# Performance work log

Hardware: AMD Instinct MI355X
Metric: run time of the kernel (lower is better)

Reference implementation:

```python
import jax, jax.numpy as jnp
import numpy as np

B, T, D = 4, 4096, 1024
HD = 64              # head_dim
H = D // HD          # n_heads = 16
C = 64               # chunk_size (T % C == 0)


def setup_inputs() -> dict:
    key = jax.random.key(0)
    k1, k2, k3 = jax.random.split(key, 3)
    out = jax.random.normal(k1, (B, T, D), jnp.float32)
    # Linear(d_model, d_model, bias=False) weights, ~1/sqrt(D) scale
    W_write = jax.random.normal(k2, (D, D), jnp.float32) * 0.03
    W_read = jax.random.normal(k3, (D, D), jnp.float32) * 0.03
    decay = jnp.full((H,), 4.6, jnp.float32)                 # torch init value
    log_alpha = jnp.log(jnp.full((H,), 0.03, jnp.float32))   # memory_alpha=0.03
    return {"out": out, "W_write": W_write, "W_read": W_read,
            "decay": decay, "log_alpha": log_alpha}


def reference(out, W_write, W_read, decay, log_alpha):
    Bb, Tt, Dd = out.shape
    d, Hh, Cc = HD, D // HD, C
    out32 = out.astype(jnp.float32)
    gamma = jax.nn.sigmoid(decay)          # (H,)
    log_gamma = jnp.log(gamma)

    # projections and head split: (B, H, T, d)
    v = (out32 @ W_write.T).reshape(Bb, Tt, Hh, d).transpose(0, 2, 1, 3)
    rk = out32.reshape(Bb, Tt, Hh, d).transpose(0, 2, 1, 3)
    wk = jnp.pad(rk[:, :, :-1], ((0, 0), (0, 0), (1, 0), (0, 0)))  # shift right by 1

    BH = Bb * Hh
    gamma_bh = jnp.tile(gamma, Bb)          # (BH,) index b*H+h -> gamma[h]
    log_gamma_bh = jnp.tile(log_gamma, Bb)
    nC = Tt // Cc
    # (nC, BH, C, d) so lax.scan runs over chunks
    v_ch = v.reshape(BH, nC, Cc, d).transpose(1, 0, 2, 3)
    rk_ch = rk.reshape(BH, nC, Cc, d).transpose(1, 0, 2, 3)
    wk_ch = wk.reshape(BH, nC, Cc, d).transpose(1, 0, 2, 3)

    p = jnp.arange(Cc)
    diffs = jnp.clip(p[:, None] - 1 - p[None, :], 0)          # (C, C)
    causal = p[:, None] > p[None, :]
    # per-(b,h) intra-chunk decay mask (BH, C, C)
    M = jnp.exp(diffs[None].astype(jnp.float32) * log_gamma_bh[:, None, None]) * causal[None]
    g_p = gamma_bh[:, None] ** p[None, :].astype(jnp.float32)            # (BH, C)
    g_w = gamma_bh[:, None] ** (Cc - 1 - p)[None, :].astype(jnp.float32)  # (BH, C)
    g_C = gamma_bh ** Cc                                                  # (BH,)

    def scan_fn(W, chunk):
        rk_c, wk_c, v_c = chunk                                   # each (BH, C, d)
        inter = jnp.einsum('bij,bcj->bci', W, rk_c) * g_p[:, :, None]
        S = jnp.einsum('bcd,bkd->bck', rk_c, wk_c)                # (BH, C, C)
        intra = jnp.einsum('bck,bkd->bcd', S * M, v_c)
        W_new = g_C[:, None, None] * W + jnp.einsum('bci,bcj->bij', v_c * g_w[:, :, None], wk_c)
        return W_new, inter + intra

    W0 = jnp.zeros((BH, d, d), jnp.float32)
    _, reads = jax.lax.scan(scan_fn, W0, (rk_ch, wk_ch, v_ch))   # (nC, BH, C, d)
    reads = reads.transpose(1, 0, 2, 3).reshape(Bb, Hh, Tt, d)
    alpha = jnp.exp(log_alpha)[None, :, None, None]
    reads = (alpha * reads).transpose(0, 2, 1, 3).reshape(Bb, Tt, Dd)
    return out + (reads @ W_read.T).astype(out.dtype)
```

## Files before the change

kernel.cpp:

```cpp
#include <hip/hip_runtime.h>
#include <hip/hip_bf16.h>
#include <stdint.h>


typedef __bf16 bf16x8 __attribute__((ext_vector_type(8)));
typedef float f32x4 __attribute__((ext_vector_type(4)));

#define GAS __attribute__((address_space(1)))
#define LAS __attribute__((address_space(3)))

__device__ __forceinline__ unsigned short f2bf(float f) {
  unsigned u = __float_as_uint(f);
  u = (u + 0x7fffu + ((u >> 16) & 1u)) >> 16;
  return (unsigned short)u;
}
__device__ __forceinline__ float bf2f(unsigned short h) {
  return __uint_as_float(((unsigned)h) << 16);
}

__global__ __launch_bounds__(256) void cast_f32_to_bf16(
    const float* __restrict__ src, unsigned short* __restrict__ dst, int n8) {
  int i = blockIdx.x * 256 + threadIdx.x;
  if (i >= n8) return;
  const float4* s = (const float4*)src + (size_t)i * 2;
  float4 f0 = s[0], f1 = s[1];
  union { uint4 u4; unsigned short us[8]; } o;
  o.us[0] = f2bf(f0.x); o.us[1] = f2bf(f0.y); o.us[2] = f2bf(f0.z); o.us[3] = f2bf(f0.w);
  o.us[4] = f2bf(f1.x); o.us[5] = f2bf(f1.y); o.us[6] = f2bf(f1.z); o.us[7] = f2bf(f1.w);
  ((uint4*)dst)[i] = o.u4;
}

__global__ __launch_bounds__(256) void cast_weights(
    const float* __restrict__ w1, const float* __restrict__ w2,
    unsigned short* __restrict__ dst) {
  int i = blockIdx.x * 256 + threadIdx.x;
  const float* src = (i < 131072) ? w1 : w2;
  int j = (i < 131072) ? i : i - 131072;
  const float4* s = (const float4*)src + (size_t)j * 2;
  float4 f0 = s[0], f1 = s[1];
  union { uint4 u4; unsigned short us[8]; } o;
  o.us[0] = f2bf(f0.x); o.us[1] = f2bf(f0.y); o.us[2] = f2bf(f0.z); o.us[3] = f2bf(f0.w);
  o.us[4] = f2bf(f1.x); o.us[5] = f2bf(f1.y); o.us[6] = f2bf(f1.z); o.us[7] = f2bf(f1.w);
  ((uint4*)dst)[i] = o.u4;
}

__device__ __forceinline__ void swizzle_bm_bn(int id, int& bm, int& bn) {
  int x = id & 7;
  int s = id >> 3;
  bn = s & 7;
  bm = ((s >> 3) << 3) | x;
}

#define STAGE4(Adst, Bdst, kofs)                                                            \
  _Pragma("unroll") for (int q = 0; q < 2; q++) {                                           \
    int g = (w * 2 + q) * 16 + lr;                                                          \
    __builtin_amdgcn_global_load_lds((GAS void*)(void*)(Ab + (size_t)g * K + (kofs) + lc),  \
                                     (LAS void*)((Adst) + (w * 2 + q) * 512), 16, 0, 0);    \
    __builtin_amdgcn_global_load_lds((GAS void*)(void*)(Bb + (size_t)g * K + (kofs) + lc),  \
                                     (LAS void*)((Bdst) + (w * 2 + q) * 512), 16, 0, 0);    \
  }

__global__ __launch_bounds__(256, 4) void gemm_bt_bf16out(
    const unsigned short* __restrict__ A, const unsigned short* __restrict__ B,
    unsigned short* __restrict__ C, int M, int N, int K) {
  __shared__ unsigned short As[4][128 * 32];
  __shared__ unsigned short Bs[4][128 * 32];
  int tid = threadIdx.x;
  int l = tid & 63, w = tid >> 6;
  int bm, bn;
  swizzle_bm_bn(blockIdx.x, bm, bn);
  int wm = (w >> 1) * 64, wn = (w & 1) * 64;
  f32x4 acc[4][4];
#pragma unroll
  for (int mi = 0; mi < 4; mi++)
#pragma unroll
    for (int ni = 0; ni < 4; ni++) acc[mi][ni] = (f32x4){0.f, 0.f, 0.f, 0.f};
  const unsigned short* Ab = A + (size_t)bm * 128 * K;
  const unsigned short* Bb = B + (size_t)bn * 128 * K;
  int lr = l >> 2, lc = (l & 3) * 8;
  int lm = l & 15, q4 = l >> 4;
  const int nit = K >> 5;
#pragma unroll
  for (int t = 0; t < 3; t++) STAGE4(&As[t][0], &Bs[t][0], t << 5)
  for (int it = 0; it < nit; it++) {
    __builtin_amdgcn_s_barrier();
    if (it + 3 < nit) {
      int t = it + 3;
      STAGE4(&As[t & 3][0], &Bs[t & 3][0], t << 5)
    }
    int rem = nit - 1 - it;
    if (rem >= 3)      asm volatile("s_waitcnt vmcnt(12)" ::: "memory");
    else if (rem == 2) asm volatile("s_waitcnt vmcnt(8)" ::: "memory");
    else if (rem == 1) asm volatile("s_waitcnt vmcnt(4)" ::: "memory");
    else               asm volatile("s_waitcnt vmcnt(0)" ::: "memory");
    __builtin_amdgcn_s_barrier();
    __builtin_amdgcn_sched_barrier(0);
    int buf = it & 3;
    bf16x8 a[4], b[4];
#pragma unroll
    for (int mi = 0; mi < 4; mi++) a[mi] = *(const bf16x8*)&As[buf][(wm + mi * 16 + lm) * 32 + q4 * 8];
#pragma unroll
    for (int ni = 0; ni < 4; ni++) b[ni] = *(const bf16x8*)&Bs[buf][(wn + ni * 16 + lm) * 32 + q4 * 8];
#pragma unroll
    for (int mi = 0; mi < 4; mi++)
#pragma unroll
      for (int ni = 0; ni < 4; ni++)
        acc[mi][ni] = __builtin_amdgcn_mfma_f32_16x16x32_bf16(a[mi], b[ni], acc[mi][ni], 0, 0, 0);
  }
#pragma unroll
  for (int mi = 0; mi < 4; mi++)
#pragma unroll
    for (int ni = 0; ni < 4; ni++) {
      int r0 = bm * 128 + wm + mi * 16 + q4 * 4;
      int col = bn * 128 + wn + ni * 16 + lm;
#pragma unroll
      for (int j = 0; j < 4; j++)
        C[(size_t)(r0 + j) * N + col] = f2bf(acc[mi][ni][j]);
    }
}

__global__ __launch_bounds__(256, 4) void gemm_bt_addout(
    const unsigned short* __restrict__ A, const unsigned short* __restrict__ B,
    const unsigned short* __restrict__ base_bf, float* __restrict__ C, int M, int N, int K) {
  __shared__ unsigned short As[4][128 * 32];
  __shared__ unsigned short Bs[4][128 * 32];
  int tid = threadIdx.x;
  int l = tid & 63, w = tid >> 6;
  int bm, bn;
  swizzle_bm_bn(blockIdx.x, bm, bn);
  int wm = (w >> 1) * 64, wn = (w & 1) * 64;
  int lr = l >> 2, lc = (l & 3) * 8;
  int lm = l & 15, q4 = l >> 4;
  const unsigned short* Ab = A + (size_t)bm * 128 * K;
  const unsigned short* Bb = B + (size_t)bn * 128 * K;
  const int nit = K >> 5;
#pragma unroll
  for (int t = 0; t < 3; t++) STAGE4(&As[t][0], &Bs[t][0], t << 5)
  f32x4 acc[4][4];
#pragma unroll
  for (int mi = 0; mi < 4; mi++)
#pragma unroll
    for (int ni = 0; ni < 4; ni++) {
      int r0 = bm * 128 + wm + mi * 16 + q4 * 4;
      int col = bn * 128 + wn + ni * 16 + lm;
#pragma unroll
      for (int j = 0; j < 4; j++)
        acc[mi][ni][j] = bf2f(base_bf[(size_t)(r0 + j) * N + col]);
    }
  for (int it = 0; it < nit; it++) {
    __builtin_amdgcn_s_barrier();
    if (it + 3 < nit) {
      int t = it + 3;
      STAGE4(&As[t & 3][0], &Bs[t & 3][0], t << 5)
    }
    int rem = nit - 1 - it;
    if (rem >= 3)      asm volatile("s_waitcnt vmcnt(12)" ::: "memory");
    else if (rem == 2) asm volatile("s_waitcnt vmcnt(8)" ::: "memory");
    else if (rem == 1) asm volatile("s_waitcnt vmcnt(4)" ::: "memory");
    else               asm volatile("s_waitcnt vmcnt(0)" ::: "memory");
    __builtin_amdgcn_s_barrier();
    __builtin_amdgcn_sched_barrier(0);
    int buf = it & 3;
    bf16x8 a[4], b[4];
#pragma unroll
    for (int mi = 0; mi < 4; mi++) a[mi] = *(const bf16x8*)&As[buf][(wm + mi * 16 + lm) * 32 + q4 * 8];
#pragma unroll
    for (int ni = 0; ni < 4; ni++) b[ni] = *(const bf16x8*)&Bs[buf][(wn + ni * 16 + lm) * 32 + q4 * 8];
#pragma unroll
    for (int mi = 0; mi < 4; mi++)
#pragma unroll
      for (int ni = 0; ni < 4; ni++)
        acc[mi][ni] = __builtin_amdgcn_mfma_f32_16x16x32_bf16(a[mi], b[ni], acc[mi][ni], 0, 0, 0);
  }
#pragma unroll
  for (int mi = 0; mi < 4; mi++)
#pragma unroll
    for (int ni = 0; ni < 4; ni++) {
      int r0 = bm * 128 + wm + mi * 16 + q4 * 4;
      int col = bn * 128 + wn + ni * 16 + lm;
#pragma unroll
      for (int j = 0; j < 4; j++)
        C[(size_t)(r0 + j) * N + col] = acc[mi][ni][j];
    }
}

__global__ __launch_bounds__(256) void chunk_local(
    const unsigned short* __restrict__ rkg,
    const unsigned short* __restrict__ vg,
    const float* __restrict__ decay,
    unsigned short* __restrict__ intra_bf,
    unsigned short* __restrict__ U_bf) {
  int c = blockIdx.x, bh = blockIdx.y;
  int b = bh >> 4, h = bh & 15;
  int tid = threadIdx.x, l = tid & 63, w = tid >> 6;
  float gamma = 1.0f / (1.0f + __expf(-decay[h]));
  float lg = __logf(gamma);

  __shared__ unsigned short rk_s[64 * 72];
  __shared__ unsigned short wk_s[64 * 72];
  __shared__ unsigned short wkT_s[64 * 72];
  __shared__ unsigned short vT_s[64 * 72];
  __shared__ unsigned short S_s[64 * 72];

  const size_t rowbase = (((size_t)b * 4096 + (size_t)c * 64) * 1024) + h * 64;

#pragma unroll
  for (int r = 0; r < 2; r++) {
    int e = r * 256 + tid;
    int p = e >> 3, seg = e & 7;
    uint4 dr = *(const uint4*)(rkg + rowbase + (size_t)p * 1024 + seg * 8);
    *(uint4*)&rk_s[p * 72 + seg * 8] = dr;
    uint4 dv = *(const uint4*)(vg + rowbase + (size_t)p * 1024 + seg * 8);
    {
      unsigned uu[4] = {dv.x, dv.y, dv.z, dv.w};
#pragma unroll
      for (int qq = 0; qq < 4; qq++) {
        vT_s[(seg * 8 + qq * 2) * 72 + p] = (unsigned short)(uu[qq] & 0xffffu);
        vT_s[(seg * 8 + qq * 2 + 1) * 72 + p] = (unsigned short)(uu[qq] >> 16);
      }
    }
    int tg = c * 64 + p - 1;
    uint4 dw = make_uint4(0u, 0u, 0u, 0u);
    if (tg >= 0) dw = *(const uint4*)(rkg + ((size_t)b * 4096 + tg) * 1024 + h * 64 + seg * 8);
    *(uint4*)&wk_s[p * 72 + seg * 8] = dw;
    {
      unsigned uu[4] = {dw.x, dw.y, dw.z, dw.w};
#pragma unroll
      for (int qq = 0; qq < 4; qq++) {
        wkT_s[(seg * 8 + qq * 2) * 72 + p] = (unsigned short)(uu[qq] & 0xffffu);
        wkT_s[(seg * 8 + qq * 2 + 1) * 72 + p] = (unsigned short)(uu[qq] >> 16);
      }
    }
  }
  __syncthreads();

  int lm = l & 15, q4 = l >> 4;

  {
    bf16x8 a0 = *(const bf16x8*)&rk_s[(w * 16 + lm) * 72 + q4 * 8];
    bf16x8 a1 = *(const bf16x8*)&rk_s[(w * 16 + lm) * 72 + 32 + q4 * 8];
#pragma unroll
    for (int ni = 0; ni < 4; ni++) {
      bf16x8 b0 = *(const bf16x8*)&wk_s[(ni * 16 + lm) * 72 + q4 * 8];
      bf16x8 b1 = *(const bf16x8*)&wk_s[(ni * 16 + lm) * 72 + 32 + q4 * 8];
      f32x4 acc = {0.f, 0.f, 0.f, 0.f};
      acc = __builtin_amdgcn_mfma_f32_16x16x32_bf16(a0, b0, acc, 0, 0, 0);
      acc = __builtin_amdgcn_mfma_f32_16x16x32_bf16(a1, b1, acc, 0, 0, 0);
#pragma unroll
      for (int j = 0; j < 4; j++) {
        int p = w * 16 + q4 * 4 + j;
        int q = ni * 16 + lm;
        float m = (p > q) ? __expf(lg * (float)(p - 1 - q)) : 0.0f;
        S_s[p * 72 + q] = f2bf(acc[j] * m);
      }
    }
  }
  __syncthreads();

  {
    bf16x8 a0 = *(const bf16x8*)&S_s[(w * 16 + lm) * 72 + q4 * 8];
    bf16x8 a1 = *(const bf16x8*)&S_s[(w * 16 + lm) * 72 + 32 + q4 * 8];
#pragma unroll
    for (int ni = 0; ni < 4; ni++) {
      bf16x8 b0 = *(const bf16x8*)&vT_s[(ni * 16 + lm) * 72 + q4 * 8];
      bf16x8 b1 = *(const bf16x8*)&vT_s[(ni * 16 + lm) * 72 + 32 + q4 * 8];
      f32x4 acc = {0.f, 0.f, 0.f, 0.f};
      acc = __builtin_amdgcn_mfma_f32_16x16x32_bf16(a0, b0, acc, 0, 0, 0);
      acc = __builtin_amdgcn_mfma_f32_16x16x32_bf16(a1, b1, acc, 0, 0, 0);
#pragma unroll
      for (int j = 0; j < 4; j++) {
        int p = w * 16 + q4 * 4 + j;
        int i = ni * 16 + lm;
        intra_bf[rowbase + (size_t)p * 1024 + i] = f2bf(acc[j]);
      }
    }
  }

  {
    bf16x8 a0 = *(const bf16x8*)&vT_s[(w * 16 + lm) * 72 + q4 * 8];
    bf16x8 a1 = *(const bf16x8*)&vT_s[(w * 16 + lm) * 72 + 32 + q4 * 8];
#pragma unroll
    for (int jj = 0; jj < 8; jj++) {
      int p0 = q4 * 8 + jj;
      a0[jj] = (__bf16)((float)a0[jj] * __expf(lg * (float)(63 - p0)));
      a1[jj] = (__bf16)((float)a1[jj] * __expf(lg * (float)(63 - (p0 + 32))));
    }
    size_t ub = ((size_t)bh * 64 + c) * 4096;
#pragma unroll
    for (int nj = 0; nj < 4; nj++) {
      bf16x8 b0 = *(const bf16x8*)&wkT_s[(nj * 16 + lm) * 72 + q4 * 8];
      bf16x8 b1 = *(const bf16x8*)&wkT_s[(nj * 16 + lm) * 72 + 32 + q4 * 8];
      f32x4 acc = {0.f, 0.f, 0.f, 0.f};
      acc = __builtin_amdgcn_mfma_f32_16x16x32_bf16(a0, b0, acc, 0, 0, 0);
      acc = __builtin_amdgcn_mfma_f32_16x16x32_bf16(a1, b1, acc, 0, 0, 0);
#pragma unroll
      for (int j = 0; j < 4; j++) {
        int i = w * 16 + q4 * 4 + j;
        int col = nj * 16 + lm;
        U_bf[ub + i * 64 + col] = f2bf(acc[j]);
      }
    }
  }
}

__global__ __launch_bounds__(256) void scan_w(
    const unsigned short* __restrict__ U_bf, const float* __restrict__ decay,
    unsigned short* __restrict__ Wst) {
  int nsl = blockIdx.x, bh = blockIdx.y;
  int h = bh & 15;
  float gamma = 1.0f / (1.0f + __expf(-decay[h]));
  float gC = __expf(64.0f * __logf(gamma));
  int n0 = nsl * 512 + threadIdx.x * 2;
  const unsigned short* Ub = U_bf + (size_t)bh * 64 * 4096 + n0;
  unsigned short* Wb = Wst + (size_t)bh * 64 * 4096 + n0;
  float w0 = 0.f, w1 = 0.f;
#pragma unroll
  for (int c = 0; c < 64; c++) {
    unsigned u = *(const unsigned*)(Ub + (size_t)c * 4096);
    ushort2 sv;
    sv.x = f2bf(w0);
    sv.y = f2bf(w1);
    *(ushort2*)(Wb + (size_t)c * 4096) = sv;
    w0 = gC * w0 + bf2f((unsigned short)(u & 0xffffu));
    w1 = gC * w1 + bf2f((unsigned short)(u >> 16));
  }
}

__global__ __launch_bounds__(256) void inter_combine(
    const unsigned short* __restrict__ rkg, const unsigned short* __restrict__ Wst,
    const unsigned short* __restrict__ intra_bf,
    const float* __restrict__ decay, const float* __restrict__ log_alpha,
    unsigned short* __restrict__ reads_bf) {
  int c = blockIdx.x, bh = blockIdx.y;
  int b = bh >> 4, h = bh & 15;
  int tid = threadIdx.x, l = tid & 63, w = tid >> 6;
  int lm = l & 15, q4 = l >> 4;
  float gamma = 1.0f / (1.0f + __expf(-decay[h]));
  float lg = __logf(gamma);
  float alpha = __expf(log_alpha[h]);

  __shared__ unsigned short rk_s[64 * 72];
  __shared__ unsigned short W_s[64 * 72];
  __shared__ unsigned short in_s[64 * 72];

  const size_t rowbase = (((size_t)b * 4096 + (size_t)c * 64) * 1024) + h * 64;
  const size_t wbase = ((size_t)bh * 64 + c) * 4096;

#pragma unroll
  for (int r = 0; r < 2; r++) {
    int e = r * 256 + tid;
    int p = e >> 3, seg = (e & 7) * 8;
    *(uint4*)&rk_s[p * 72 + seg] = *(const uint4*)(rkg + rowbase + (size_t)p * 1024 + seg);
    *(uint4*)&in_s[p * 72 + seg] = *(const uint4*)(intra_bf + rowbase + (size_t)p * 1024 + seg);
    *(uint4*)&W_s[p * 72 + seg] = *(const uint4*)(Wst + wbase + (size_t)p * 64 + seg);
  }
  __syncthreads();

  bf16x8 a0 = *(const bf16x8*)&rk_s[(w * 16 + lm) * 72 + q4 * 8];
  bf16x8 a1 = *(const bf16x8*)&rk_s[(w * 16 + lm) * 72 + 32 + q4 * 8];
#pragma unroll
  for (int ni = 0; ni < 4; ni++) {
    bf16x8 b0 = *(const bf16x8*)&W_s[(ni * 16 + lm) * 72 + q4 * 8];
    bf16x8 b1 = *(const bf16x8*)&W_s[(ni * 16 + lm) * 72 + 32 + q4 * 8];
    f32x4 acc = {0.f, 0.f, 0.f, 0.f};
    acc = __builtin_amdgcn_mfma_f32_16x16x32_bf16(a0, b0, acc, 0, 0, 0);
    acc = __builtin_amdgcn_mfma_f32_16x16x32_bf16(a1, b1, acc, 0, 0, 0);
#pragma unroll
    for (int j = 0; j < 4; j++) {
      int p = w * 16 + q4 * 4 + j;
      int i = ni * 16 + lm;
      float gp = __expf(lg * (float)p);
      reads_bf[rowbase + (size_t)p * 1024 + i] =
          f2bf(alpha * (acc[j] * gp + bf2f(in_s[p * 72 + i])));
    }
  }
}

extern "C" void kernel_launch(void* const* d_in, const int* in_sizes, int n_in,
                              void* d_out, int out_size, void* d_ws, size_t ws_size,
                              hipStream_t stream) {
  const float* out_f = (const float*)d_in[0];
  const float* Ww = (const float*)d_in[1];
  const float* Wr = (const float*)d_in[2];
  const float* decay = (const float*)d_in[3];
  const float* lalpha = (const float*)d_in[4];

  char* ws = (char*)d_ws;
  unsigned short* outbf = (unsigned short*)(ws + 0);
  unsigned short* vbf   = (unsigned short*)(ws + 33554432);
  unsigned short* wwbf  = (unsigned short*)(ws + 67108864);
  unsigned short* wrbf  = (unsigned short*)(ws + 69206016);
  unsigned short* intra = (unsigned short*)(ws + 71303168);
  unsigned short* U     = (unsigned short*)(ws + 104857600);
  unsigned short* Wst   = (unsigned short*)(ws + 138412032);
  unsigned short* reads = (unsigned short*)(ws + 171966464);

  cast_f32_to_bf16<<<dim3(8192), 256, 0, stream>>>(out_f, outbf, 16777216 / 8);
  cast_weights<<<dim3(1024), 256, 0, stream>>>(Ww, Wr, wwbf);

  gemm_bt_bf16out<<<dim3(1024), 256, 0, stream>>>(outbf, wwbf, vbf, 16384, 1024, 1024);

  chunk_local<<<dim3(64, 64), 256, 0, stream>>>(outbf, vbf, decay, intra, U);

  scan_w<<<dim3(8, 64), 256, 0, stream>>>(U, decay, Wst);
  inter_combine<<<dim3(64, 64), 256, 0, stream>>>(outbf, Wst, intra, decay, lalpha, reads);

  gemm_bt_addout<<<dim3(1024), 256, 0, stream>>>(reads, wrbf, outbf, (float*)d_out,
                                                 16384, 1024, 1024);
}
```

Measured before the change: 303.6 us.

## Replace both GEMMs with a 256x256-tile, 512-thread ping-pong pipelined kernel

```diff
diff --git a/kernel.cpp b/kernel.cpp
--- a/kernel.cpp
+++ b/kernel.cpp
@@ -44,144 +44,140 @@
   ((uint4*)dst)[i] = o.u4;
 }
 
-__device__ __forceinline__ void swizzle_bm_bn(int id, int& bm, int& bn) {
-  int x = id & 7;
-  int s = id >> 3;
-  bn = s & 7;
-  bm = ((s >> 3) << 3) | x;
-}
-
-#define STAGE4(Adst, Bdst, kofs)                                                            \
-  _Pragma("unroll") for (int q = 0; q < 2; q++) {                                           \
-    int g = (w * 2 + q) * 16 + lr;                                                          \
-    __builtin_amdgcn_global_load_lds((GAS void*)(void*)(Ab + (size_t)g * K + (kofs) + lc),  \
-                                     (LAS void*)((Adst) + (w * 2 + q) * 512), 16, 0, 0);    \
-    __builtin_amdgcn_global_load_lds((GAS void*)(void*)(Bb + (size_t)g * K + (kofs) + lc),  \
-                                     (LAS void*)((Bdst) + (w * 2 + q) * 512), 16, 0, 0);    \
-  }
-
-__global__ __launch_bounds__(256, 4) void gemm_bt_bf16out(
+
+#define STG(XB, SLOT, HIDX, HF, KT)                                                  \
+  do {                                                                               \
+    if ((KT) < nT) {                                                                 \
+      _Pragma("unroll") for (int r_ = 0; r_ < 2; r_++)                               \
+          __builtin_amdgcn_global_load_lds(                                          \
+              (GAS void*)(void*)((XB) +                                              \
+                                 (size_t)((HF) * 128 + (tid >> 3) + r_ * 64) * K +   \
+                                 ((KT) << 6) + srcc),                                \
+              (LAS void*)(&lds[SLOT][HIDX][w64 * 512 + r_ * 4096]), 16, 0, 0);       \
+    }                                                                                \
+  } while (0)
+
+#define DSRA(SLOT, MH)                                                               \
+  _Pragma("unroll") for (int m_ = 0; m_ < 4; m_++)                                   \
+  _Pragma("unroll") for (int ks_ = 0; ks_ < 2; ks_++)                                \
+      a[m_][ks_] = *(const bf16x8*)&lds[SLOT][aH][((MH) * 64 + m_ * 16 + lm) * 64 +  \
+                                                  ((ks_ * 32 + q4 * 8) ^ swz)];
+
+#define DSRB(SLOT, BB, N0)                                                           \
+  _Pragma("unroll") for (int n_ = 0; n_ < 2; n_++)                                   \
+  _Pragma("unroll") for (int ks_ = 0; ks_ < 2; ks_++)                                \
+      BB[n_][ks_] = *(const bf16x8*)&lds[SLOT][bH][(brow0 + ((N0) + n_) * 16 + lm) * 64 + \
+                                                   ((ks_ * 32 + q4 * 8) ^ swz)];
+
+#define MMA(MH, BB, N0)                                                              \
+  __builtin_amdgcn_s_setprio(1);                                                     \
+  _Pragma("unroll") for (int m_ = 0; m_ < 4; m_++)                                   \
+  _Pragma("unroll") for (int n_ = 0; n_ < 2; n_++)                                   \
+  _Pragma("unroll") for (int ks_ = 0; ks_ < 2; ks_++)                                \
+      acc[(MH) * 4 + m_][(N0) + n_] = __builtin_amdgcn_mfma_f32_16x16x32_bf16(       \
+          a[m_][ks_], BB[n_][ks_], acc[(MH) * 4 + m_][(N0) + n_], 0, 0, 0);          \
+  __builtin_amdgcn_s_setprio(0);
+
+#define BARW                                                                         \
+  __builtin_amdgcn_s_barrier();                                                      \
+  asm volatile("s_waitcnt lgkmcnt(0)" ::: "memory");                                 \
+  __builtin_amdgcn_sched_barrier(0);
+
+#define BARE                                                                         \
+  __builtin_amdgcn_s_barrier();                                                      \
+  __builtin_amdgcn_sched_barrier(0);
+
+template <bool ADD>
+__global__ __launch_bounds__(512, 2) void gemm256(
     const unsigned short* __restrict__ A, const unsigned short* __restrict__ B,
-    unsigned short* __restrict__ C, int M, int N, int K) {
-  __shared__ unsigned short As[4][128 * 32];
-  __shared__ unsigned short Bs[4][128 * 32];
+    const unsigned short* __restrict__ base_bf, void* __restrict__ Cout,
+    int M, int N, int K) {
+  __shared__ unsigned short lds[2][4][8192];
   int tid = threadIdx.x;
-  int l = tid & 63, w = tid >> 6;
-  int bm, bn;
-  swizzle_bm_bn(blockIdx.x, bm, bn);
-  int wm = (w >> 1) * 64, wn = (w & 1) * 64;
-  f32x4 acc[4][4];
-#pragma unroll
-  for (int mi = 0; mi < 4; mi++)
-#pragma unroll
-    for (int ni = 0; ni < 4; ni++) acc[mi][ni] = (f32x4){0.f, 0.f, 0.f, 0.f};
-  const unsigned short* Ab = A + (size_t)bm * 128 * K;
-  const unsigned short* Bb = B + (size_t)bn * 128 * K;
-  int lr = l >> 2, lc = (l & 3) * 8;
+  int l = tid & 63, w64 = tid >> 6;
   int lm = l & 15, q4 = l >> 4;
-  const int nit = K >> 5;
-#pragma unroll
-  for (int t = 0; t < 3; t++) STAGE4(&As[t][0], &Bs[t][0], t << 5)
-  for (int it = 0; it < nit; it++) {
-    __builtin_amdgcn_s_barrier();
-    if (it + 3 < nit) {
-      int t = it + 3;
-      STAGE4(&As[t & 3][0], &Bs[t & 3][0], t << 5)
-    }
-    int rem = nit - 1 - it;
-    if (rem >= 3)      asm volatile("s_waitcnt vmcnt(12)" ::: "memory");
-    else if (rem == 2) asm volatile("s_waitcnt vmcnt(8)" ::: "memory");
-    else if (rem == 1) asm volatile("s_waitcnt vmcnt(4)" ::: "memory");
-    else               asm volatile("s_waitcnt vmcnt(0)" ::: "memory");
-    __builtin_amdgcn_s_barrier();
-    __builtin_amdgcn_sched_barrier(0);
-    int buf = it & 3;
-    bf16x8 a[4], b[4];
-#pragma unroll
-    for (int mi = 0; mi < 4; mi++) a[mi] = *(const bf16x8*)&As[buf][(wm + mi * 16 + lm) * 32 + q4 * 8];
-#pragma unroll
-    for (int ni = 0; ni < 4; ni++) b[ni] = *(const bf16x8*)&Bs[buf][(wn + ni * 16 + lm) * 32 + q4 * 8];
-#pragma unroll
-    for (int mi = 0; mi < 4; mi++)
-#pragma unroll
-      for (int ni = 0; ni < 4; ni++)
-        acc[mi][ni] = __builtin_amdgcn_mfma_f32_16x16x32_bf16(a[mi], b[ni], acc[mi][ni], 0, 0, 0);
-  }
-#pragma unroll
-  for (int mi = 0; mi < 4; mi++)
-#pragma unroll
-    for (int ni = 0; ni < 4; ni++) {
-      int r0 = bm * 128 + wm + mi * 16 + q4 * 4;
-      int col = bn * 128 + wn + ni * 16 + lm;
-#pragma unroll
-      for (int j = 0; j < 4; j++)
-        C[(size_t)(r0 + j) * N + col] = f2bf(acc[mi][ni][j]);
-    }
-}
-
-__global__ __launch_bounds__(256, 4) void gemm_bt_addout(
-    const unsigned short* __restrict__ A, const unsigned short* __restrict__ B,
-    const unsigned short* __restrict__ base_bf, float* __restrict__ C, int M, int N, int K) {
-  __shared__ unsigned short As[4][128 * 32];
-  __shared__ unsigned short Bs[4][128 * 32];
-  int tid = threadIdx.x;
-  int l = tid & 63, w = tid >> 6;
-  int bm, bn;
-  swizzle_bm_bn(blockIdx.x, bm, bn);
-  int wm = (w >> 1) * 64, wn = (w & 1) * 64;
-  int lr = l >> 2, lc = (l & 3) * 8;
-  int lm = l & 15, q4 = l >> 4;
-  const unsigned short* Ab = A + (size_t)bm * 128 * K;
-  const unsigned short* Bb = B + (size_t)bn * 128 * K;
-  const int nit = K >> 5;
-#pragma unroll
-  for (int t = 0; t < 3; t++) STAGE4(&As[t][0], &Bs[t][0], t << 5)
-  f32x4 acc[4][4];
-#pragma unroll
-  for (int mi = 0; mi < 4; mi++)
-#pragma unroll
-    for (int ni = 0; ni < 4; ni++) {
-      int r0 = bm * 128 + wm + mi * 16 + q4 * 4;
-      int col = bn * 128 + wn + ni * 16 + lm;
-#pragma unroll
-      for (int j = 0; j < 4; j++)
-        acc[mi][ni][j] = bf2f(base_bf[(size_t)(r0 + j) * N + col]);
-    }
-  for (int it = 0; it < nit; it++) {
-    __builtin_amdgcn_s_barrier();
-    if (it + 3 < nit) {
-      int t = it + 3;
-      STAGE4(&As[t & 3][0], &Bs[t & 3][0], t << 5)
-    }
-    int rem = nit - 1 - it;
-    if (rem >= 3)      asm volatile("s_waitcnt vmcnt(12)" ::: "memory");
-    else if (rem == 2) asm volatile("s_waitcnt vmcnt(8)" ::: "memory");
-    else if (rem == 1) asm volatile("s_waitcnt vmcnt(4)" ::: "memory");
-    else               asm volatile("s_waitcnt vmcnt(0)" ::: "memory");
-    __builtin_amdgcn_s_barrier();
-    __builtin_amdgcn_sched_barrier(0);
-    int buf = it & 3;
-    bf16x8 a[4], b[4];
-#pragma unroll
-    for (int mi = 0; mi < 4; mi++) a[mi] = *(const bf16x8*)&As[buf][(wm + mi * 16 + lm) * 32 + q4 * 8];
-#pragma unroll
-    for (int ni = 0; ni < 4; ni++) b[ni] = *(const bf16x8*)&Bs[buf][(wn + ni * 16 + lm) * 32 + q4 * 8];
-#pragma unroll
-    for (int mi = 0; mi < 4; mi++)
-#pragma unroll
-      for (int ni = 0; ni < 4; ni++)
-        acc[mi][ni] = __builtin_amdgcn_mfma_f32_16x16x32_bf16(a[mi], b[ni], acc[mi][ni], 0, 0, 0);
-  }
-#pragma unroll
-  for (int mi = 0; mi < 4; mi++)
-#pragma unroll
-    for (int ni = 0; ni < 4; ni++) {
-      int r0 = bm * 128 + wm + mi * 16 + q4 * 4;
-      int col = bn * 128 + wn + ni * 16 + lm;
-#pragma unroll
-      for (int j = 0; j < 4; j++)
-        C[(size_t)(r0 + j) * N + col] = acc[mi][ni][j];
-    }
+  int swz = ((lm >> 2) & 1) << 5;
+  int srcc = ((tid & 7) * 8) ^ (((tid >> 5) & 1) << 5);
+  int aH = w64 >> 2;
+  int bH = 2 + ((w64 & 3) >> 1);
+  int brow0 = (w64 & 1) * 64;
+  int id = blockIdx.x;
+  int xcd = id & 7, s = id >> 3;
+  int bn = s & 3, bm = (s >> 2) * 8 + xcd;
+  const unsigned short* Ab = A + (size_t)bm * 256 * K;
+  const unsigned short* Bb = B + (size_t)bn * 256 * K;
+  const int nT = K >> 6, nI = nT >> 1;
+
+  STG(Bb, 0, 2, 0, 0); STG(Bb, 0, 3, 1, 0);
+  STG(Ab, 0, 0, 0, 0); STG(Ab, 0, 1, 1, 0);
+  STG(Bb, 1, 2, 0, 1); STG(Bb, 1, 3, 1, 1);
+  asm volatile("s_waitcnt vmcnt(4)" ::: "memory");
+  __builtin_amdgcn_s_barrier();
+  __builtin_amdgcn_sched_barrier(0);
+
+  f32x4 acc[8][4];
+  if constexpr (ADD) {
+#pragma unroll
+    for (int mh = 0; mh < 2; mh++)
+#pragma unroll
+      for (int m = 0; m < 4; m++)
+#pragma unroll
+        for (int nf = 0; nf < 4; nf++) {
+          int r0 = bm * 256 + (w64 >> 2) * 128 + mh * 64 + m * 16 + q4 * 4;
+          int col = bn * 256 + (w64 & 3) * 64 + nf * 16 + lm;
+#pragma unroll
+          for (int j = 0; j < 4; j++)
+            acc[mh * 4 + m][nf][j] = bf2f(base_bf[(size_t)(r0 + j) * N + col]);
+        }
+  } else {
+#pragma unroll
+    for (int mf = 0; mf < 8; mf++)
+#pragma unroll
+      for (int nf = 0; nf < 4; nf++) acc[mf][nf] = (f32x4){0.f, 0.f, 0.f, 0.f};
+  }
+
+  bf16x8 a[4][2], b0[2][2], b1[2][2];
+  for (int i = 0; i < nI; i++) {
+    int t1 = 2 * i + 1, t2 = 2 * i + 2, t3 = 2 * i + 3;
+    DSRA(0, 0); DSRB(0, b0, 0); STG(Ab, 1, 0, 0, t1);
+    BARW; MMA(0, b0, 0); BARE;
+    DSRB(0, b1, 2); STG(Ab, 1, 1, 1, t1);
+    BARW; MMA(0, b1, 2); BARE;
+    DSRA(0, 1); STG(Bb, 0, 2, 0, t2);
+    BARW; MMA(1, b1, 2); BARE;
+    STG(Bb, 0, 3, 1, t2);
+    BARW; MMA(1, b0, 0);
+    if (i < nI - 1) { asm volatile("s_waitcnt vmcnt(4)" ::: "memory"); }
+    else            { asm volatile("s_waitcnt vmcnt(0)" ::: "memory"); }
+    BARE;
+    DSRA(1, 0); DSRB(1, b0, 0); STG(Ab, 0, 0, 0, t2);
+    BARW; MMA(0, b0, 0); BARE;
+    DSRB(1, b1, 2); STG(Ab, 0, 1, 1, t2);
+    BARW; MMA(0, b1, 2); BARE;
+    DSRA(1, 1); STG(Bb, 1, 2, 0, t3);
+    BARW; MMA(1, b1, 2); BARE;
+    STG(Bb, 1, 3, 1, t3);
+    BARW; MMA(1, b0, 0);
+    if (i < nI - 1) { asm volatile("s_waitcnt vmcnt(4)" ::: "memory"); }
+    BARE;
+  }
+
+#pragma unroll
+  for (int mh = 0; mh < 2; mh++)
+#pragma unroll
+    for (int m = 0; m < 4; m++)
+#pragma unroll
+      for (int nf = 0; nf < 4; nf++) {
+        int r0 = bm * 256 + (w64 >> 2) * 128 + mh * 64 + m * 16 + q4 * 4;
+        int col = bn * 256 + (w64 & 3) * 64 + nf * 16 + lm;
+#pragma unroll
+        for (int j = 0; j < 4; j++) {
+          if constexpr (ADD)
+            ((float*)Cout)[(size_t)(r0 + j) * N + col] = acc[mh * 4 + m][nf][j];
+          else
+            ((unsigned short*)Cout)[(size_t)(r0 + j) * N + col] = f2bf(acc[mh * 4 + m][nf][j]);
+        }
+      }
 }
 
 __global__ __launch_bounds__(256) void chunk_local(
@@ -398,13 +394,12 @@
   cast_f32_to_bf16<<<dim3(8192), 256, 0, stream>>>(out_f, outbf, 16777216 / 8);
   cast_weights<<<dim3(1024), 256, 0, stream>>>(Ww, Wr, wwbf);
 
-  gemm_bt_bf16out<<<dim3(1024), 256, 0, stream>>>(outbf, wwbf, vbf, 16384, 1024, 1024);
+  gemm256<false><<<dim3(256), 512, 0, stream>>>(outbf, wwbf, nullptr, vbf, 16384, 1024, 1024);
 
   chunk_local<<<dim3(64, 64), 256, 0, stream>>>(outbf, vbf, decay, intra, U);
 
   scan_w<<<dim3(8, 64), 256, 0, stream>>>(U, decay, Wst);
   inter_combine<<<dim3(64, 64), 256, 0, stream>>>(outbf, Wst, intra, decay, lalpha, reads);
 
-  gemm_bt_addout<<<dim3(1024), 256, 0, stream>>>(reads, wrbf, outbf, (float*)d_out,
-                                                 16384, 1024, 1024);
-}
+  gemm256<true><<<dim3(256), 512, 0, stream>>>(reads, wrbf, outbf, d_out, 16384, 1024, 1024);
+}
```

Measured after the change: 285.1 us. -6.1%, faster.
